# Optimization experiments

Measured on AMD Instinct MI355X. Metric: run time of the kernel, lower is better.

Reference implementation:

```python
import jax, jax.numpy as jnp
import numpy as np

GAUSS_START = 0.5
GAUSS_END = 5.0
N_GAUSS = 16
N_ATOMS = 3072
N_GRAPHS = 64
K_GRID = 4096


def setup_inputs() -> dict:
    key = jax.random.key(0)
    k1, k2, k3, k4 = jax.random.split(key, 4)
    coeff = jax.random.normal(k1, (N_ATOMS, N_GAUSS), dtype=jnp.float32)
    atom_coord = jax.random.normal(k2, (N_ATOMS, 3), dtype=jnp.float32)
    grid = jax.random.normal(k3, (N_GRAPHS, K_GRID, 3), dtype=jnp.float32)
    batch = jnp.sort(jax.random.randint(k4, (N_ATOMS,), 0, N_GRAPHS, dtype=jnp.int64))
    return {"coeff": coeff, "atom_coord": atom_coord, "grid": grid, "batch": batch}


def reference(coeff, atom_coord, grid, batch):
    # Precomputed gaussian widths (buffers in the torch module)
    sigma = jnp.linspace(GAUSS_START, GAUSS_END, N_GAUSS, dtype=jnp.float32)
    sigma_r = 1.0 / (sigma * np.float32(np.sqrt(2.0 * np.pi))) ** 3  # (n_gauss,)
    sigma_2r = 1.0 / sigma ** 2  # (n_gauss,)

    # Gather per-atom grid: (N, K, 3)
    sample_vec = grid[batch] - atom_coord[:, None, :]
    r2 = jnp.sum(sample_vec ** 2, axis=-1)  # (N, K)
    # Gaussian basis on grid: (N, K, n_gauss)
    orbital = jnp.exp(-r2[..., None] * sigma_2r) * sigma_r
    # Weighted sum over gaussians: (N, K)
    density = jnp.einsum('nkg,ng->nk', orbital, coeff)
    # Scatter-add atoms back to their graph: (G, K)
    return jax.ops.segment_sum(density, batch, num_segments=N_GRAPHS)
```

## Files before the change

### kernel.cpp

```cpp
#include <hip/hip_runtime.h>
#include <cmath>

constexpr int N_GAUSS = 16;
constexpr int N_GRAPHS = 64;
constexpr int K_GRID = 4096;

constexpr int NSEG = 512;
constexpr int TSTRIDE = 528;
constexpr float RMAX = 12.0f;

constexpr int KCHUNK = 256;
constexpr int KPER = 4;
constexpr int KSPAN = KCHUNK * KPER;
constexpr int CHUNKS = K_GRID / KSPAN;
constexpr int APB = 12;

struct GaussParams {
    float ns2[N_GAUSS];
    float b[N_GAUSS];
};

__device__ __forceinline__ float fast_exp2(float x) {
    return __builtin_amdgcn_exp2f(x);
}

__global__ __launch_bounds__(256) void build_table_kernel(
    const float* __restrict__ coeff,
    float* __restrict__ table,
    float* __restrict__ out,
    GaussParams p)
{
    const int a = blockIdx.y;
    const int t = (int)threadIdx.x;
    const int n = blockIdx.x * 256 + t;

    if (blockIdx.x == 0 && a < (N_GRAPHS * K_GRID) / (256 * 4)) {
        ((float4*)out)[a * 256 + t] = make_float4(0.f, 0.f, 0.f, 0.f);
    }

    const float* __restrict__ cf = coeff + a * N_GAUSS;

    auto eval = [&](int idx) -> float {
        if (idx > NSEG) return 0.f;
        const float r = (float)idx * (RMAX / (float)NSEG);
        const float r2 = r * r;
        float a0 = 0.f, a1 = 0.f, a2 = 0.f, a3 = 0.f;
        #pragma unroll
        for (int g = 0; g < N_GAUSS; g += 4) {
            a0 = fmaf(cf[g + 0], fast_exp2(fmaf(r2, p.ns2[g + 0], p.b[g + 0])), a0);
            a1 = fmaf(cf[g + 1], fast_exp2(fmaf(r2, p.ns2[g + 1], p.b[g + 1])), a1);
            a2 = fmaf(cf[g + 2], fast_exp2(fmaf(r2, p.ns2[g + 2], p.b[g + 2])), a2);
            a3 = fmaf(cf[g + 3], fast_exp2(fmaf(r2, p.ns2[g + 3], p.b[g + 3])), a3);
        }
        return (a0 + a1) + (a2 + a3);
    };

    table[(size_t)a * TSTRIDE + n] = eval(n);
    if (blockIdx.x == 1 && t < TSTRIDE - 512) {
        const int n2 = 512 + t;
        table[(size_t)a * TSTRIDE + n2] = eval(n2);
    }
}

__global__ __launch_bounds__(KCHUNK) void GaussianOrbital_kernel(
    const float* __restrict__ table,
    const float* __restrict__ atom_coord,
    const float* __restrict__ grid,
    const int* __restrict__ batch,
    float* __restrict__ out,
    int n_atoms)
{
    __shared__ float lds[APB * TSTRIDE];

    const int chunk = blockIdx.x;
    const int ablk  = blockIdx.y;
    const int t = (int)threadIdx.x;

    const int lo = ablk * APB;
    int hi = lo + APB; if (hi > n_atoms) hi = n_atoms;

    {
        const float4* __restrict__ src = (const float4*)(table + (size_t)lo * TSTRIDE);
        float4* dst = (float4*)lds;
        const int nvec = (hi - lo) * TSTRIDE / 4;
        #pragma unroll 2
        for (int i = t; i < nvec; i += KCHUNK) dst[i] = src[i];
    }
    __syncthreads();

    int cur_g = __builtin_amdgcn_readfirstlane(batch[lo]);

    float kx[KPER], ky[KPER], kz[KPER], acc[KPER];
    auto load_grid = [&](int g) {
        #pragma unroll
        for (int j = 0; j < KPER; ++j) {
            const int k = chunk * KSPAN + j * KCHUNK + t;
            const int b = (g * K_GRID + k) * 3;
            kx[j] = grid[b + 0]; ky[j] = grid[b + 1]; kz[j] = grid[b + 2];
        }
    };
    auto flush = [&](int g) {
        #pragma unroll
        for (int j = 0; j < KPER; ++j) {
            const int k = chunk * KSPAN + j * KCHUNK + t;
            atomicAdd(&out[g * K_GRID + k], acc[j]);
            acc[j] = 0.f;
        }
    };
    load_grid(cur_g);
    #pragma unroll
    for (int j = 0; j < KPER; ++j) acc[j] = 0.f;

    for (int a = lo; a < hi; ++a) {
        const int g = __builtin_amdgcn_readfirstlane(batch[a]);
        if (g != cur_g) {
            flush(cur_g);
            cur_g = g;
            load_grid(cur_g);
        }

        const float ax = atom_coord[a * 3 + 0];
        const float ay = atom_coord[a * 3 + 1];
        const float az = atom_coord[a * 3 + 2];
        const float* __restrict__ T = lds + (a - lo) * TSTRIDE;

        float fr[KPER]; int ii[KPER];
        #pragma unroll
        for (int j = 0; j < KPER; ++j) {
            const float dx = kx[j] - ax, dy = ky[j] - ay, dz = kz[j] - az;
            const float r2 = fmaf(dx, dx, fmaf(dy, dy, dz * dz));
            float tt = __builtin_amdgcn_sqrtf(r2) * ((float)NSEG / RMAX);
            tt = fminf(tt, (float)(NSEG - 1));
            const int i = (int)tt;
            fr[j] = tt - (float)i;
            ii[j] = i;
        }
        float f0[KPER], f1[KPER];
        #pragma unroll
        for (int j = 0; j < KPER; ++j) { f0[j] = T[ii[j]]; f1[j] = T[ii[j] + 1]; }
        #pragma unroll
        for (int j = 0; j < KPER; ++j) acc[j] = acc[j] + fmaf(fr[j], f1[j] - f0[j], f0[j]);
    }

    flush(cur_g);
}

extern "C" void kernel_launch(void* const* d_in, const int* in_sizes, int n_in,
                              void* d_out, int out_size, void* d_ws, size_t ws_size,
                              hipStream_t stream)
{
    const float* coeff      = (const float*)d_in[0];
    const float* atom_coord = (const float*)d_in[1];
    const float* grid       = (const float*)d_in[2];
    const int*   batch      = (const int*)d_in[3];
    float* out   = (float*)d_out;
    float* table = (float*)d_ws;
    const int n_atoms = in_sizes[0] / N_GAUSS;

    GaussParams p;
    const double sqrt2pi = 2.50662827463100050242;
    for (int g = 0; g < N_GAUSS; ++g) {
        const double sigma = 0.5 + (5.0 - 0.5) * (double)g / (double)(N_GAUSS - 1);
        p.ns2[g] = (float)(-1.44269504088896340736 / (sigma * sigma));
        const double sr = 1.0 / (sigma * sqrt2pi * sigma * sqrt2pi * sigma * sqrt2pi);
        p.b[g] = (float)(std::log2(sr));
    }

    {
        dim3 gDim(2, n_atoms);
        hipLaunchKernelGGL(build_table_kernel, gDim, dim3(256), 0, stream,
                           coeff, table, out, p);
    }
    {
        const int n_ablk = (n_atoms + APB - 1) / APB;
        dim3 gDim(CHUNKS, n_ablk);
        hipLaunchKernelGGL(GaussianOrbital_kernel, gDim, dim3(KCHUNK), 0, stream,
                           table, atom_coord, grid, batch, out, n_atoms);
    }
}
```

Measured before the change: 82.42 us.

## Parallelize over graphs with segment offsets instead of atom blocks with atomics

Replaces the atom-block decomposition, which used atomicAdd flushes into a pre-zeroed output, with one block per (graph, k-chunk). Each block loops over that graph's atoms, found by a binary search of segment starts in the table kernel, and writes its output once with no atomics. This removes the output zeroing, the atomic traffic and the reloading of grid points on graph changes. In exchange the number of atoms per block varies with graph size, each thread handles only one grid point, and table tiles are reloaded into LDS per 16 atoms with extra barriers.

```diff
diff --git a/kernel.cpp b/kernel.cpp
--- a/kernel.cpp
+++ b/kernel.cpp
@@ -9,11 +9,9 @@
 constexpr int TSTRIDE = 528;
 constexpr float RMAX = 12.0f;
 
-constexpr int KCHUNK = 256;
-constexpr int KPER = 4;
-constexpr int KSPAN = KCHUNK * KPER;
-constexpr int CHUNKS = K_GRID / KSPAN;
-constexpr int APB = 12;
+constexpr int TPB2 = 256;
+constexpr int CHUNKS2 = K_GRID / TPB2;
+constexpr int ATILE = 16;
 
 struct GaussParams {
     float ns2[N_GAUSS];
@@ -26,16 +24,23 @@
 
 __global__ __launch_bounds__(256) void build_table_kernel(
     const float* __restrict__ coeff,
+    const int*   __restrict__ batch,
     float* __restrict__ table,
-    float* __restrict__ out,
-    GaussParams p)
+    int*   __restrict__ gstart,
+    GaussParams p, int n_atoms)
 {
     const int a = blockIdx.y;
     const int t = (int)threadIdx.x;
     const int n = blockIdx.x * 256 + t;
 
-    if (blockIdx.x == 0 && a < (N_GRAPHS * K_GRID) / (256 * 4)) {
-        ((float4*)out)[a * 256 + t] = make_float4(0.f, 0.f, 0.f, 0.f);
+    if (blockIdx.x == 0 && a == 0 && t <= N_GRAPHS) {
+        const int g = t;
+        int lo = 0, hi = n_atoms;
+        while (lo < hi) {
+            const int mid = (lo + hi) >> 1;
+            if (batch[mid] < g) lo = mid + 1; else hi = mid;
+        }
+        gstart[t] = lo;
     }
 
     const float* __restrict__ cf = coeff + a * N_GAUSS;
@@ -62,87 +67,77 @@
     }
 }
 
-__global__ __launch_bounds__(KCHUNK) void GaussianOrbital_kernel(
+__global__ __launch_bounds__(TPB2, 4) void GaussianOrbital_kernel(
     const float* __restrict__ table,
     const float* __restrict__ atom_coord,
     const float* __restrict__ grid,
-    const int* __restrict__ batch,
-    float* __restrict__ out,
-    int n_atoms)
+    const int*   __restrict__ gstart,
+    float* __restrict__ out)
 {
-    __shared__ float lds[APB * TSTRIDE];
+    __shared__ float lds[ATILE * TSTRIDE];
 
-    const int chunk = blockIdx.x;
-    const int ablk  = blockIdx.y;
+    const int g = blockIdx.y;
     const int t = (int)threadIdx.x;
+    const int k = blockIdx.x * TPB2 + t;
 
-    const int lo = ablk * APB;
-    int hi = lo + APB; if (hi > n_atoms) hi = n_atoms;
+    const int s = __builtin_amdgcn_readfirstlane(gstart[g]);
+    const int e = __builtin_amdgcn_readfirstlane(gstart[g + 1]);
 
-    {
-        const float4* __restrict__ src = (const float4*)(table + (size_t)lo * TSTRIDE);
-        float4* dst = (float4*)lds;
-        const int nvec = (hi - lo) * TSTRIDE / 4;
-        #pragma unroll 2
-        for (int i = t; i < nvec; i += KCHUNK) dst[i] = src[i];
-    }
-    __syncthreads();
+    const int b = (g * K_GRID + k) * 3;
+    const float kx = grid[b + 0], ky = grid[b + 1], kz = grid[b + 2];
 
-    int cur_g = __builtin_amdgcn_readfirstlane(batch[lo]);
+    float acc0 = 0.f, acc1 = 0.f;
 
-    float kx[KPER], ky[KPER], kz[KPER], acc[KPER];
-    auto load_grid = [&](int g) {
-        #pragma unroll
-        for (int j = 0; j < KPER; ++j) {
-            const int k = chunk * KSPAN + j * KCHUNK + t;
-            const int b = (g * K_GRID + k) * 3;
-            kx[j] = grid[b + 0]; ky[j] = grid[b + 1]; kz[j] = grid[b + 2];
+    auto body = [&](const float* __restrict__ T,
+                    float ax, float ay, float az, float& acc) {
+        const float dx = kx - ax, dy = ky - ay, dz = kz - az;
+        const float r2 = fmaf(dx, dx, fmaf(dy, dy, dz * dz));
+        float tt = __builtin_amdgcn_sqrtf(r2) * ((float)NSEG / RMAX);
+        tt = fminf(tt, (float)(NSEG - 1));
+        const int i = (int)tt;
+        const float fr = tt - (float)i;
+        const float f0 = T[i], f1 = T[i + 1];
+        acc += fmaf(fr, f1 - f0, f0);
+    };
+
+    for (int a0 = s; a0 < e; a0 += ATILE) {
+        const int na = min(ATILE, e - a0);
+
+        __syncthreads();
+        {
+            const float4* __restrict__ src =
+                (const float4*)(table + (size_t)a0 * TSTRIDE);
+            float4* dst = (float4*)lds;
+            const int nvec = na * (TSTRIDE / 4);
+            for (int i = t; i < nvec; i += TPB2) dst[i] = src[i];
         }
-    };
-    auto flush = [&](int g) {
-        #pragma unroll
-        for (int j = 0; j < KPER; ++j) {
-            const int k = chunk * KSPAN + j * KCHUNK + t;
-            atomicAdd(&out[g * K_GRID + k], acc[j]);
-            acc[j] = 0.f;
+        __syncthreads();
+
+        if (na == ATILE) {
+            float axs[ATILE], ays[ATILE], azs[ATILE];
+            #pragma unroll
+            for (int u = 0; u < ATILE; ++u) {
+                const int a = a0 + u;
+                axs[u] = atom_coord[a * 3 + 0];
+                ays[u] = atom_coord[a * 3 + 1];
+                azs[u] = atom_coord[a * 3 + 2];
+            }
+            #pragma unroll
+            for (int u = 0; u < ATILE; ++u) {
+                body(lds + u * TSTRIDE, axs[u], ays[u], azs[u],
+                     (u & 1) ? acc1 : acc0);
+            }
+        } else {
+            for (int u = 0; u < na; ++u) {
+                const int a = a0 + u;
+                body(lds + u * TSTRIDE,
+                     atom_coord[a * 3 + 0], atom_coord[a * 3 + 1],
+                     atom_coord[a * 3 + 2], (u & 1) ? acc1 : acc0);
+            }
         }
-    };
-    load_grid(cur_g);
-    #pragma unroll
-    for (int j = 0; j < KPER; ++j) acc[j] = 0.f;
-
-    for (int a = lo; a < hi; ++a) {
-        const int g = __builtin_amdgcn_readfirstlane(batch[a]);
-        if (g != cur_g) {
-            flush(cur_g);
-            cur_g = g;
-            load_grid(cur_g);
-        }
-
-        const float ax = atom_coord[a * 3 + 0];
-        const float ay = atom_coord[a * 3 + 1];
-        const float az = atom_coord[a * 3 + 2];
-        const float* __restrict__ T = lds + (a - lo) * TSTRIDE;
-
-        float fr[KPER]; int ii[KPER];
-        #pragma unroll
-        for (int j = 0; j < KPER; ++j) {
-            const float dx = kx[j] - ax, dy = ky[j] - ay, dz = kz[j] - az;
-            const float r2 = fmaf(dx, dx, fmaf(dy, dy, dz * dz));
-            float tt = __builtin_amdgcn_sqrtf(r2) * ((float)NSEG / RMAX);
-            tt = fminf(tt, (float)(NSEG - 1));
-            const int i = (int)tt;
-            fr[j] = tt - (float)i;
-            ii[j] = i;
-        }
-        float f0[KPER], f1[KPER];
-        #pragma unroll
-        for (int j = 0; j < KPER; ++j) { f0[j] = T[ii[j]]; f1[j] = T[ii[j] + 1]; }
-        #pragma unroll
-        for (int j = 0; j < KPER; ++j) acc[j] = acc[j] + fmaf(fr[j], f1[j] - f0[j], f0[j]);
     }
 
-    flush(cur_g);
+    out[g * K_GRID + k] = acc0 + acc1;
 }
 
 extern "C" void kernel_launch(void* const* d_in, const int* in_sizes, int n_in,
@@ -156,6 +151,7 @@
     float* out   = (float*)d_out;
     float* table = (float*)d_ws;
     const int n_atoms = in_sizes[0] / N_GAUSS;
+    int* gstart = (int*)(table + (size_t)n_atoms * TSTRIDE);
 
     GaussParams p;
     const double sqrt2pi = 2.50662827463100050242;
@@ -169,12 +165,11 @@
     {
         dim3 gDim(2, n_atoms);
         hipLaunchKernelGGL(build_table_kernel, gDim, dim3(256), 0, stream,
-                           coeff, table, out, p);
+                           coeff, batch, table, gstart, p, n_atoms);
     }
     {
-        const int n_ablk = (n_atoms + APB - 1) / APB;
-        dim3 gDim(CHUNKS, n_ablk);
-        hipLaunchKernelGGL(GaussianOrbital_kernel, gDim, dim3(KCHUNK), 0, stream,
-                           table, atom_coord, grid, batch, out, n_atoms);
+        dim3 gDim(CHUNKS2, N_GRAPHS);
+        hipLaunchKernelGGL(GaussianOrbital_kernel, gDim, dim3(TPB2), 0, stream,
+                           table, atom_coord, grid, gstart, out);
     }
 }
```

Result: slower. 86.80 us (+5.3%).
